# Optimization experiments

Hardware: AMD Instinct MI355X
Metric: run time of the kernel (lower is better)

The kernel has to match this reference:

```python
import jax, jax.numpy as jnp
import numpy as np

B, G, T, C = 32, 4, 512, 256


def setup_inputs() -> dict:
    key = jax.random.key(0)
    k1, k2, k3 = jax.random.split(key, 3)
    x = jax.random.normal(k1, (B, G, T, C), dtype=jnp.float32)
    # learned per-channel params, initialized around the repo defaults 0.3 / 0.1
    w_input = 0.3 * jax.random.uniform(k2, (C,), dtype=jnp.float32) + 0.15
    w_leak = 0.1 * jax.random.uniform(k3, (C,), dtype=jnp.float32) + 0.05
    return {"x": x, "w_input": w_input, "w_leak": w_leak}


def _heaviside(v):
    # theta_forget: step function with zero gradient (matches @tf.custom_gradient)
    return jax.lax.stop_gradient((v >= 0).astype(v.dtype))


def reference(x, w_input, w_leak):
    # x: (B, G, T, C) -> flatten group into batch, scan over time
    b, g, t, c = x.shape
    V_THRESH = 1.0   # V_thresh default
    T_REF = 1.0      # t_refrectory receives self.thresh (=1) positionally
    xr = jnp.transpose(x.reshape(b * g, t, c), (1, 0, 2))  # (T, N, C)

    def step(carry, xt):
        Vm, R = carry
        R = _heaviside(Vm - V_THRESH) * T_REF + _heaviside(R - 1.0) * (R - 1.0)
        Vm = (w_input * xt + (1.0 - w_leak) * Vm) * _heaviside(-R)
        return (Vm, R), Vm

    zeros = jnp.zeros((b * g, c), dtype=x.dtype)
    _, Vs = jax.lax.scan(step, (zeros, zeros), xr)  # Vs: (T, N, C)
    return jnp.transpose(Vs, (1, 0, 2)).reshape(b, g, t, c)
```

## Files before the change

### kernel.cpp

```cpp
#include <hip/hip_runtime.h>


constexpr int T_STEPS = 512;
constexpr int CCH     = 256;
constexpr int NSEQ    = 128;
constexpr int D       = 32;
constexpr int CB      = 64;

__global__ __launch_bounds__(64, 1) void lif_kernel(
    const float* __restrict__ x,
    const float* __restrict__ w_input,
    const float* __restrict__ w_leak,
    float* __restrict__ out)
{
#pragma clang fp contract(off)
    __shared__ float obuf[4 * CB];

    const int lane = threadIdx.x;
    const int b    = blockIdx.x;
    const int n  = (b & 7) + ((b >> 5) << 3);
    const int cb = ((b >> 3) & 3) << 6;

    const int ch = cb + lane;
    const float w = w_input[ch];
    const float a = 1.0f - w_leak[ch];

    const float* xp = x + (size_t)n * T_STEPS * CCH + ch;
    float* go = out + (size_t)n * T_STEPS * CCH + cb + (lane >> 4) * CCH + 4 * (lane & 15);

    float buf[D];
#pragma unroll
    for (int d0 = 0; d0 < D; ++d0) buf[d0] = xp[(size_t)d0 * CCH];

    float Vm = 0.0f;

    for (int t0 = 0; t0 < T_STEPS - D; t0 += D) {
#pragma unroll
        for (int k = 0; k < D; ++k) {
            const float xt = buf[k];
            buf[k] = xp[(size_t)(t0 + D + k) * CCH];

            const float v = (w * xt) + (a * Vm);
            Vm = (Vm - 1.0f >= 0.0f) ? 0.0f : v;

            obuf[(k & 3) * CB + lane] = Vm;
            if ((k & 3) == 3) {
                const float4 vv = *(const float4*)&obuf[(lane >> 4) * CB + 4 * (lane & 15)];
                *(float4*)(go + (size_t)(t0 + (k - 3)) * CCH) = vv;
            }
        }
    }

#pragma unroll
    for (int k = 0; k < D; ++k) {
        const float xt = buf[k];
        const float v = (w * xt) + (a * Vm);
        Vm = (Vm - 1.0f >= 0.0f) ? 0.0f : v;

        obuf[(k & 3) * CB + lane] = Vm;
        if ((k & 3) == 3) {
            const float4 vv = *(const float4*)&obuf[(lane >> 4) * CB + 4 * (lane & 15)];
            *(float4*)(go + (size_t)(T_STEPS - D + (k - 3)) * CCH) = vv;
        }
    }
}

extern "C" void kernel_launch(void* const* d_in, const int* in_sizes, int n_in,
                              void* d_out, int out_size, void* d_ws, size_t ws_size,
                              hipStream_t stream) {
    const float* x       = (const float*)d_in[0];
    const float* w_input = (const float*)d_in[1];
    const float* w_leak  = (const float*)d_in[2];
    float* out = (float*)d_out;

    dim3 grid(NSEQ * (CCH / CB));
    dim3 block(64);
    hipLaunchKernelGGL(lif_kernel, grid, block, 0, stream,
                       x, w_input, w_leak, out);
}
```

Before: 30.76 us.

## Use one 256-thread block per sequence with double-buffered LDS output windows

The grid changes from 512 single-wavefront blocks (64 channels each) to 128 blocks of 256 threads, each covering all channels of one sequence. Each window of 32 timesteps is written into a double-buffered LDS tile [2][32][256]. The previous window is then flushed as coalesced float4 rows spread over the four waves, overlapping with computation of the next window, and a barrier separates windows. This is meant to replace the per-4-step wave-local shuffle and store with bulk full-row stores and overlapped writeback. The cost is a block-wide barrier per window and fewer blocks (128) than CUs on the device.

```diff
diff --git a/kernel.cpp b/kernel.cpp
--- a/kernel.cpp
+++ b/kernel.cpp
@@ -1,68 +1,78 @@
 #include <hip/hip_runtime.h>
 
+
+typedef float f32x4 __attribute__((ext_vector_type(4)));
 
 constexpr int T_STEPS = 512;
 constexpr int CCH     = 256;
 constexpr int NSEQ    = 128;
-constexpr int D       = 32;
-constexpr int CB      = 64;
+constexpr int WIN     = 32;
+constexpr int NWIN    = T_STEPS / WIN;
 
-__global__ __launch_bounds__(64, 1) void lif_kernel(
+__device__ __forceinline__ void window_barrier() {
+    __builtin_amdgcn_sched_barrier(0);
+    asm volatile("s_waitcnt lgkmcnt(0)" ::: "memory");
+    __builtin_amdgcn_s_barrier();
+    __builtin_amdgcn_sched_barrier(0);
+}
+
+__global__ __launch_bounds__(256, 1) void lif_kernel(
     const float* __restrict__ x,
     const float* __restrict__ w_input,
     const float* __restrict__ w_leak,
     float* __restrict__ out)
 {
 #pragma clang fp contract(off)
-    __shared__ float obuf[4 * CB];
+    __shared__ float obuf[2][WIN][CCH];
 
-    const int lane = threadIdx.x;
-    const int b    = blockIdx.x;
-    const int n  = (b & 7) + ((b >> 5) << 3);
-    const int cb = ((b >> 3) & 3) << 6;
+    const int j  = threadIdx.x;
+    const int wv = j >> 6;
+    const int l  = j & 63;
+    const int n  = blockIdx.x;
 
-    const int ch = cb + lane;
-    const float w = w_input[ch];
-    const float a = 1.0f - w_leak[ch];
+    const float w = w_input[j];
+    const float a = 1.0f - w_leak[j];
 
-    const float* xp = x + (size_t)n * T_STEPS * CCH + ch;
-    float* go = out + (size_t)n * T_STEPS * CCH + cb + (lane >> 4) * CCH + 4 * (lane & 15);
+    const float* xp = x + (size_t)n * T_STEPS * CCH + j;
+    float* ob = out + (size_t)n * T_STEPS * CCH + 4 * l;
 
-    float buf[D];
+    float buf[WIN];
 #pragma unroll
-    for (int d0 = 0; d0 < D; ++d0) buf[d0] = xp[(size_t)d0 * CCH];
+    for (int k = 0; k < WIN; ++k) buf[k] = xp[(size_t)k * CCH];
 
     float Vm = 0.0f;
 
-    for (int t0 = 0; t0 < T_STEPS - D; t0 += D) {
+    auto do_stores = [&](int p, int tbase) {
 #pragma unroll
-        for (int k = 0; k < D; ++k) {
+        for (int s = 0; s < 8; ++s) {
+            const int r = s * 4 + wv;
+            const f32x4 vv = *(const f32x4*)&obuf[p][r][4 * l];
+            *(f32x4*)(ob + (size_t)(tbase + r) * CCH) = vv;
+        }
+    };
+
+    auto do_window = [&](int p, int t0, bool refill) {
+#pragma unroll
+        for (int k = 0; k < WIN; ++k) {
             const float xt = buf[k];
-            buf[k] = xp[(size_t)(t0 + D + k) * CCH];
-
+            if (refill) buf[k] = xp[(size_t)(t0 + WIN + k) * CCH];
             const float v = (w * xt) + (a * Vm);
             Vm = (Vm - 1.0f >= 0.0f) ? 0.0f : v;
+            obuf[p][k][j] = Vm;
+        }
+    };
 
-            obuf[(k & 3) * CB + lane] = Vm;
-            if ((k & 3) == 3) {
-                const float4 vv = *(const float4*)&obuf[(lane >> 4) * CB + 4 * (lane & 15)];
-                *(float4*)(go + (size_t)(t0 + (k - 3)) * CCH) = vv;
-            }
-        }
+    do_window(0, 0, true);
+    window_barrier();
+    for (int W = 1; W < NWIN - 1; ++W) {
+        do_stores((W - 1) & 1, (W - 1) * WIN);
+        do_window(W & 1, W * WIN, true);
+        window_barrier();
     }
-
-#pragma unroll
-    for (int k = 0; k < D; ++k) {
-        const float xt = buf[k];
-        const float v = (w * xt) + (a * Vm);
-        Vm = (Vm - 1.0f >= 0.0f) ? 0.0f : v;
-
-        obuf[(k & 3) * CB + lane] = Vm;
-        if ((k & 3) == 3) {
-            const float4 vv = *(const float4*)&obuf[(lane >> 4) * CB + 4 * (lane & 15)];
-            *(float4*)(go + (size_t)(T_STEPS - D + (k - 3)) * CCH) = vv;
-        }
-    }
+    do_stores((NWIN - 2) & 1, (NWIN - 2) * WIN);
+    do_window((NWIN - 1) & 1, (NWIN - 1) * WIN, false);
+    window_barrier();
+    do_stores((NWIN - 1) & 1, (NWIN - 1) * WIN);
 }
 
 extern "C" void kernel_launch(void* const* d_in, const int* in_sizes, int n_in,
@@ -73,8 +83,8 @@
     const float* w_leak  = (const float*)d_in[2];
     float* out = (float*)d_out;
 
-    dim3 grid(NSEQ * (CCH / CB));
-    dim3 block(64);
+    dim3 grid(NSEQ);
+    dim3 block(CCH);
     hipLaunchKernelGGL(lif_kernel, grid, block, 0, stream,
                        x, w_input, w_leak, out);
 }
```

After: 30.26 us. About the same (-1.6%).

## Process four channels per lane with float4 loads/stores and explicit schedule barriers

Applied to the files above, without the earlier changes.

Each lane now owns four adjacent channels and uses vectorized float4 loads and stores directly, with no LDS transpose buffer. Each block therefore covers all 256 channels of one sequence, and the grid shrinks from 512 to 128 blocks. Sched barriers order prefetch, compute and store in chunks of 8 rows, so four independent recurrences run interleaved per lane to hide the serial dependency. The cost is fewer wavefronts on the GPU (128 single-wave blocks) and four times the register buffer per lane, which can lower memory-level parallelism.

```diff
diff --git a/kernel.cpp b/kernel.cpp
--- a/kernel.cpp
+++ b/kernel.cpp
@@ -1,11 +1,21 @@
 #include <hip/hip_runtime.h>
 
+
+typedef float f32x4 __attribute__((ext_vector_type(4)));
 
 constexpr int T_STEPS = 512;
 constexpr int CCH     = 256;
 constexpr int NSEQ    = 128;
-constexpr int D       = 32;
-constexpr int CB      = 64;
+constexpr int ROWS    = 32;
+constexpr int NIT     = T_STEPS / ROWS;
+
+__device__ __forceinline__ void sfence() { __builtin_amdgcn_sched_barrier(0); }
+
+__device__ __forceinline__ float stepf(float xt, float w, float a, float& Vm) {
+    const float v = (w * xt) + (a * Vm);
+    Vm = (Vm - 1.0f >= 0.0f) ? 0.0f : v;
+    return Vm;
+}
 
 __global__ __launch_bounds__(64, 1) void lif_kernel(
     const float* __restrict__ x,
@@ -14,53 +24,57 @@
     float* __restrict__ out)
 {
 #pragma clang fp contract(off)
-    __shared__ float obuf[4 * CB];
+    const int l = threadIdx.x;
+    const int n = blockIdx.x;
 
-    const int lane = threadIdx.x;
-    const int b    = blockIdx.x;
-    const int n  = (b & 7) + ((b >> 5) << 3);
-    const int cb = ((b >> 3) & 3) << 6;
+    const size_t base = (size_t)n * T_STEPS * CCH + 4 * l;
+    const float* xg = x   + base;
+    float*       og = out + base;
 
-    const int ch = cb + lane;
-    const float w = w_input[ch];
-    const float a = 1.0f - w_leak[ch];
+    const f32x4 w4 = *(const f32x4*)(w_input + 4 * l);
+    const f32x4 l4 = *(const f32x4*)(w_leak  + 4 * l);
+    const float w0 = w4.x, w1 = w4.y, w2 = w4.z, w3 = w4.w;
+    const float a0 = 1.0f - l4.x, a1 = 1.0f - l4.y,
+                a2 = 1.0f - l4.z, a3 = 1.0f - l4.w;
 
-    const float* xp = x + (size_t)n * T_STEPS * CCH + ch;
-    float* go = out + (size_t)n * T_STEPS * CCH + cb + (lane >> 4) * CCH + 4 * (lane & 15);
+    f32x4 buf[ROWS];
+#pragma unroll
+    for (int r = 0; r < ROWS; ++r)
+        buf[r] = *(const f32x4*)(xg + (size_t)r * CCH);
 
-    float buf[D];
+    float Vm0 = 0.0f, Vm1 = 0.0f, Vm2 = 0.0f, Vm3 = 0.0f;
+
+    for (int W = 0; W < NIT; ++W) {
+        const int tb = W * ROWS;
 #pragma unroll
-    for (int d0 = 0; d0 < D; ++d0) buf[d0] = xp[(size_t)d0 * CCH];
+        for (int cc = 0; cc < 4; ++cc) {
+            f32x4 xt[8];
+#pragma unroll
+            for (int j = 0; j < 8; ++j) xt[j] = buf[cc * 8 + j];
+            sfence();
 
-    float Vm = 0.0f;
+            if (W + 1 < NIT) {
+#pragma unroll
+                for (int j = 0; j < 8; ++j)
+                    buf[cc * 8 + j] =
+                        *(const f32x4*)(xg + (size_t)(tb + ROWS + cc * 8 + j) * CCH);
+            }
+            sfence();
 
-    for (int t0 = 0; t0 < T_STEPS - D; t0 += D) {
+            f32x4 sv[8];
 #pragma unroll
-        for (int k = 0; k < D; ++k) {
-            const float xt = buf[k];
-            buf[k] = xp[(size_t)(t0 + D + k) * CCH];
-
-            const float v = (w * xt) + (a * Vm);
-            Vm = (Vm - 1.0f >= 0.0f) ? 0.0f : v;
-
-            obuf[(k & 3) * CB + lane] = Vm;
-            if ((k & 3) == 3) {
-                const float4 vv = *(const float4*)&obuf[(lane >> 4) * CB + 4 * (lane & 15)];
-                *(float4*)(go + (size_t)(t0 + (k - 3)) * CCH) = vv;
+            for (int j = 0; j < 8; ++j) {
+                sv[j].x = stepf(xt[j].x, w0, a0, Vm0);
+                sv[j].y = stepf(xt[j].y, w1, a1, Vm1);
+                sv[j].z = stepf(xt[j].z, w2, a2, Vm2);
+                sv[j].w = stepf(xt[j].w, w3, a3, Vm3);
             }
-        }
-    }
+            sfence();
 
 #pragma unroll
-    for (int k = 0; k < D; ++k) {
-        const float xt = buf[k];
-        const float v = (w * xt) + (a * Vm);
-        Vm = (Vm - 1.0f >= 0.0f) ? 0.0f : v;
-
-        obuf[(k & 3) * CB + lane] = Vm;
-        if ((k & 3) == 3) {
-            const float4 vv = *(const float4*)&obuf[(lane >> 4) * CB + 4 * (lane & 15)];
-            *(float4*)(go + (size_t)(T_STEPS - D + (k - 3)) * CCH) = vv;
+            for (int j = 0; j < 8; ++j)
+                *(f32x4*)(og + (size_t)(tb + cc * 8 + j) * CCH) = sv[j];
+            sfence();
         }
     }
 }
@@ -73,7 +87,7 @@
     const float* w_leak  = (const float*)d_in[2];
     float* out = (float*)d_out;
 
-    dim3 grid(NSEQ * (CCH / CB));
+    dim3 grid(NSEQ);
     dim3 block(64);
     hipLaunchKernelGGL(lif_kernel, grid, block, 0, stream,
                        x, w_input, w_leak, out);
```

Result: slower. 35.00 us (+13.8%).
